# Kernel optimization log

Hardware: AMD Instinct MI355X
Metric: run time of the kernel (lower is better)

The kernel has to match this reference:

```python
import jax, jax.numpy as jnp
import numpy as np

B, ND, NE, D, H = 2, 2048, 2048, 1024, 16
HD = D // H
DFF = 4 * D
EPS = 1e-5


def setup_inputs() -> dict:
    key = jax.random.key(0)
    ks = jax.random.split(key, 16)
    s = lambda fan_in: 1.0 / np.sqrt(fan_in)
    inp = {
        'x': jax.random.normal(ks[0], (B, ND, D), jnp.float32),
        'memory': jax.random.normal(ks[1], (B, NE, D), jnp.float32),
        'ln1_g': jnp.ones((D,), jnp.float32), 'ln1_b': jnp.zeros((D,), jnp.float32),
        'Wqkv': jax.random.normal(ks[2], (D, 3 * D), jnp.float32) * s(D),
        'Wo_sa': jax.random.normal(ks[3], (D, D), jnp.float32) * s(D),
        'bo_sa': jnp.zeros((D,), jnp.float32),
        'ln2_g': jnp.ones((D,), jnp.float32), 'ln2_b': jnp.zeros((D,), jnp.float32),
        'Wq': jax.random.normal(ks[4], (D, D), jnp.float32) * s(D),
        'Wk': jax.random.normal(ks[5], (D, D), jnp.float32) * s(D),
        'Wv': jax.random.normal(ks[6], (D, D), jnp.float32) * s(D),
        'Wo_ca': jax.random.normal(ks[7], (D, D), jnp.float32) * s(D),
        'bo_ca': jnp.zeros((D,), jnp.float32),
        'ln3_g': jnp.ones((D,), jnp.float32), 'ln3_b': jnp.zeros((D,), jnp.float32),
        'W1': jax.random.normal(ks[8], (D, DFF), jnp.float32) * s(D),
        'b1': jnp.zeros((DFF,), jnp.float32),
        'W2': jax.random.normal(ks[9], (DFF, D), jnp.float32) * s(DFF),
        'b2': jnp.zeros((D,), jnp.float32),
        'attn_mask': jnp.tril(jnp.ones((ND, ND), jnp.bool_)),
    }
    return inp


def _layernorm(x, g, b):
    mu = jnp.mean(x, axis=-1, keepdims=True)
    var = jnp.mean(jnp.square(x - mu), axis=-1, keepdims=True)
    return (x - mu) * jax.lax.rsqrt(var + EPS) * g + b


def _heads(t, n):  # (B,N,D) -> (B,H,N,HD)
    Bn = t.shape[0]
    return t.reshape(Bn, n, H, HD).transpose(0, 2, 1, 3)


def _attend(q, k, v, mask=None):
    scale = HD ** -0.5
    scores = jnp.einsum('bhqd,bhkd->bhqk', q, k) * scale
    if mask is not None:
        scores = jnp.where(mask, scores, -jnp.inf)
    attn = jax.nn.softmax(scores, axis=-1)
    out = jnp.einsum('bhqk,bhkd->bhqd', attn, v)
    Bn, _, Nq, _ = out.shape
    return out.transpose(0, 2, 1, 3).reshape(Bn, Nq, D)


def reference(x, memory, ln1_g, ln1_b, Wqkv, Wo_sa, bo_sa, ln2_g, ln2_b,
              Wq, Wk, Wv, Wo_ca, bo_ca, ln3_g, ln3_b, W1, b1, W2, b2, attn_mask):
    # --- masked self-attention ---
    h = _layernorm(x, ln1_g, ln1_b)
    qkv = (h @ Wqkv).reshape(B, ND, 3, H, HD).transpose(2, 0, 3, 1, 4)  # (3,B,H,N,HD)
    q, k, v = qkv[0], qkv[1], qkv[2]
    sa = _attend(q, k, v, attn_mask[None, None]) @ Wo_sa + bo_sa
    x = x + sa
    # --- cross-attention ---
    h = _layernorm(x, ln2_g, ln2_b)
    q = _heads(h @ Wq, ND)
    k = _heads(memory @ Wk, NE)
    v = _heads(memory @ Wv, NE)
    ca = _attend(q, k, v) @ Wo_ca + bo_ca
    x = x + ca
    # --- FFN ---
    h = _layernorm(x, ln3_g, ln3_b)
    x = x + (jax.nn.gelu(h @ W1 + b1, approximate=False) @ W2 + b2)
    return x
```

## Files before the change

### kernel.cpp

```cpp
#include <hip/hip_runtime.h>
#include <hip/hip_bf16.h>
#include <math.h>

#define B_   2
#define ND_  2048
#define NE_  2048
#define D_   1024
#define H_   16
#define HD_  64
#define DFF_ 4096
#define T_   4096

typedef __attribute__((ext_vector_type(8))) short bf16x8;
typedef __attribute__((ext_vector_type(4))) float f32x4;

#if __has_builtin(__builtin_amdgcn_exp2f)
#define EXP2(x) __builtin_amdgcn_exp2f(x)
#else
#define EXP2(x) exp2f(x)
#endif

__device__ __forceinline__ short f2bf(float f) {
  union { float f; unsigned u; } v; v.f = f;
  return (short)((v.u + 0x7FFFu + ((v.u >> 16) & 1u)) >> 16);
}
__device__ __forceinline__ float bf2f(short s) {
  union { unsigned u; float f; } v; v.u = ((unsigned)(unsigned short)s) << 16;
  return v.f;
}

typedef const __attribute__((address_space(1))) void gvoid_t;
typedef __attribute__((address_space(3))) void lvoid_t;

__device__ __forceinline__ void gload16(const void* src, void* dst) {
  __builtin_amdgcn_global_load_lds((gvoid_t*)src, (lvoid_t*)dst, 16, 0, 0);
}

__global__ __launch_bounds__(256) void prep(
    const float* __restrict__ Wqkv, short* __restrict__ wqkv_t,
    const float* __restrict__ W1, short* __restrict__ w1_t,
    const float* __restrict__ W2, short* __restrict__ w2_t,
    const float* __restrict__ i0, const float* __restrict__ i1,
    const float* __restrict__ i2, const float* __restrict__ i3,
    const float* __restrict__ i4,
    short* __restrict__ o0, short* __restrict__ o1, short* __restrict__ o2,
    short* __restrict__ o3, short* __restrict__ o4,
    const float* __restrict__ mem, short* __restrict__ membf) {
  const int id = blockIdx.x;
  const int tid = threadIdx.x;
  if (id >= 16384) {
    const int i = (id - 16384) * 256 + tid;
    float4 v = ((const float4*)mem)[i];
    short4 o;
    o.x = f2bf(v.x); o.y = f2bf(v.y); o.z = f2bf(v.z); o.w = f2bf(v.w);
    ((short4*)membf)[i] = o;
    return;
  }
  const float* in; short* out; int K, N, bx, by;
  if (id < 3072) {
    in = Wqkv; out = wqkv_t; K = 1024; N = 3072; bx = id % 96; by = id / 96;
  } else if (id < 7168) {
    const int t = id - 3072;
    in = W1; out = w1_t; K = 1024; N = 4096; bx = t % 128; by = t / 128;
  } else if (id < 11264) {
    const int t = id - 7168;
    in = W2; out = w2_t; K = 4096; N = 1024; bx = t % 32; by = t / 32;
  } else {
    const int t = id - 11264;
    const int z = t >> 10, r = t & 1023;
    bx = r % 32; by = r / 32; K = 1024; N = 1024;
    in  = z == 0 ? i0 : z == 1 ? i1 : z == 2 ? i2 : z == 3 ? i3 : i4;
    out = z == 0 ? o0 : z == 1 ? o1 : z == 2 ? o2 : z == 3 ? o3 : o4;
  }
  __shared__ float tb[32][33];
  const int tx = tid & 31, ty = tid >> 5;
  const int n0 = bx * 32, k0 = by * 32;
#pragma unroll
  for (int i = 0; i < 4; ++i)
    tb[ty + i * 8][tx] = in[(size_t)(k0 + ty + i * 8) * N + n0 + tx];
  __syncthreads();
#pragma unroll
  for (int i = 0; i < 4; ++i)
    out[(size_t)(n0 + ty + i * 8) * K + k0 + tx] = f2bf(tb[tx][ty + i * 8]);
}

__global__ __launch_bounds__(256) void ln_kernel(const float* __restrict__ x,
                                                 const float* __restrict__ g,
                                                 const float* __restrict__ b,
                                                 short* __restrict__ out) {
  const int row = blockIdx.x;
  const int tid = threadIdx.x;
  const float* xr = x + (size_t)row * D_;
  float4 v = reinterpret_cast<const float4*>(xr)[tid];
  float s  = v.x + v.y + v.z + v.w;
  float s2 = v.x * v.x + v.y * v.y + v.z * v.z + v.w * v.w;
#pragma unroll
  for (int m = 1; m < 64; m <<= 1) {
    s  += __shfl_xor(s, m);
    s2 += __shfl_xor(s2, m);
  }
  __shared__ float ss[4], ss2[4];
  const int w = tid >> 6;
  if ((tid & 63) == 0) { ss[w] = s; ss2[w] = s2; }
  __syncthreads();
  s  = ss[0] + ss[1] + ss[2] + ss[3];
  s2 = ss2[0] + ss2[1] + ss2[2] + ss2[3];
  const float mu   = s * (1.0f / D_);
  const float var  = s2 * (1.0f / D_) - mu * mu;
  const float rstd = rsqrtf(var + 1e-5f);
  float4 gv = reinterpret_cast<const float4*>(g)[tid];
  float4 bv = reinterpret_cast<const float4*>(b)[tid];
  short4 o;
  o.x = f2bf((v.x - mu) * rstd * gv.x + bv.x);
  o.y = f2bf((v.y - mu) * rstd * gv.y + bv.y);
  o.z = f2bf((v.z - mu) * rstd * gv.z + bv.z);
  o.w = f2bf((v.w - mu) * rstd * gv.w + bv.w);
  reinterpret_cast<short4*>(out + (size_t)row * D_)[tid] = o;
}

__global__ __launch_bounds__(256) void ln_fused(const float* __restrict__ xprev,
                                                const short* delta,
                                                const float* __restrict__ pbias,
                                                const float* __restrict__ g,
                                                const float* __restrict__ b,
                                                short* out_ln,
                                                float* __restrict__ out_x) {
  const int row = blockIdx.x;
  const int tid = threadIdx.x;
  float4 v = reinterpret_cast<const float4*>(xprev + (size_t)row * D_)[tid];
  short4 dv = reinterpret_cast<const short4*>(delta + (size_t)row * D_)[tid];
  float4 pb = reinterpret_cast<const float4*>(pbias)[tid];
  v.x += bf2f(dv.x) + pb.x;
  v.y += bf2f(dv.y) + pb.y;
  v.z += bf2f(dv.z) + pb.z;
  v.w += bf2f(dv.w) + pb.w;
  float s  = v.x + v.y + v.z + v.w;
  float s2 = v.x * v.x + v.y * v.y + v.z * v.z + v.w * v.w;
#pragma unroll
  for (int m = 1; m < 64; m <<= 1) {
    s  += __shfl_xor(s, m);
    s2 += __shfl_xor(s2, m);
  }
  __shared__ float ss[4], ss2[4];
  const int w = tid >> 6;
  if ((tid & 63) == 0) { ss[w] = s; ss2[w] = s2; }
  __syncthreads();
  s  = ss[0] + ss[1] + ss[2] + ss[3];
  s2 = ss2[0] + ss2[1] + ss2[2] + ss2[3];
  const float mu   = s * (1.0f / D_);
  const float var  = s2 * (1.0f / D_) - mu * mu;
  const float rstd = rsqrtf(var + 1e-5f);
  reinterpret_cast<float4*>(out_x + (size_t)row * D_)[tid] = v;
  float4 gv = reinterpret_cast<const float4*>(g)[tid];
  float4 bv = reinterpret_cast<const float4*>(b)[tid];
  short4 o;
  o.x = f2bf((v.x - mu) * rstd * gv.x + bv.x);
  o.y = f2bf((v.y - mu) * rstd * gv.y + bv.y);
  o.z = f2bf((v.z - mu) * rstd * gv.z + bv.z);
  o.w = f2bf((v.w - mu) * rstd * gv.w + bv.w);
  reinterpret_cast<short4*>(out_ln + (size_t)row * D_)[tid] = o;
}

__global__ __launch_bounds__(256) void addbias(const float* __restrict__ x,
                                               const short* __restrict__ delta,
                                               const float* __restrict__ bias,
                                               float* __restrict__ out) {
  const int i = blockIdx.x * 256 + threadIdx.x;
  float4 v = ((const float4*)x)[i];
  short4 dv = ((const short4*)delta)[i];
  const int col = (i * 4) & (D_ - 1);
  float4 pb = *(const float4*)(bias + col);
  v.x += bf2f(dv.x) + pb.x;
  v.y += bf2f(dv.y) + pb.y;
  v.z += bf2f(dv.z) + pb.z;
  v.w += bf2f(dv.w) + pb.w;
  ((float4*)out)[i] = v;
}

template <int MODE>
__global__ __launch_bounds__(256) void gemm_bt(const short* __restrict__ A,
                                               const short* __restrict__ Bt,
                                               const float* __restrict__ bias,
                                               void* __restrict__ Cout,
                                               int M, int N, int K) {
  __shared__ short As[2][128 * 64];
  __shared__ short Bs[2][128 * 64];
  const int tid = threadIdx.x;
  const int gx = gridDim.x;
  const int nwg = gx * gridDim.y;
  int lin = blockIdx.y * gx + blockIdx.x;
  lin = (lin & 7) * (nwg >> 3) + (lin >> 3);
  const int m0 = (lin / gx) * 128, n0 = (lin % gx) * 128;
  const int wave = tid >> 6, lane = tid & 63;
  const int wm = (wave >> 1) * 64, wn = (wave & 1) * 64;
  const int lr = lane & 15, lg = lane >> 4;
  const int lx = lr & 7;

  f32x4 acc[4][4];
#pragma unroll
  for (int i = 0; i < 4; ++i)
#pragma unroll
    for (int j = 0; j < 4; ++j) acc[i][j] = f32x4{0.f, 0.f, 0.f, 0.f};

  const int sr = tid >> 3;
  const int scs = ((tid & 7) ^ (sr & 7)) * 8;
  const size_t arow = (size_t)(m0 + sr) * K + scs;
  const size_t brow = (size_t)(n0 + sr) * K + scs;

  auto stage = [&](int buf, int k0) {
#pragma unroll
    for (int p = 0; p < 4; ++p) {
      gload16(A + arow + (size_t)(p * 32) * K + k0, &As[buf][p * 2048 + tid * 8]);
      gload16(Bt + brow + (size_t)(p * 32) * K + k0, &Bs[buf][p * 2048 + tid * 8]);
    }
  };

  stage(0, 0);
  __syncthreads();
  int cur = 0;
  for (int k0 = 0; k0 < K; k0 += 64) {
    if (k0 + 64 < K) stage(cur ^ 1, k0 + 64);
    const short* Ab = &As[cur][0];
    const short* Bb = &Bs[cur][0];
#pragma unroll
    for (int kk = 0; kk < 2; ++kk) {
      bf16x8 af[4], bfr[4];
#pragma unroll
      for (int mi = 0; mi < 4; ++mi)
        af[mi] = *(const bf16x8*)(Ab + (wm + mi * 16 + lr) * 64 +
                                  (((kk * 4 + lg) ^ lx) * 8));
#pragma unroll
      for (int ni = 0; ni < 4; ++ni)
        bfr[ni] = *(const bf16x8*)(Bb + (wn + ni * 16 + lr) * 64 +
                                   (((kk * 4 + lg) ^ lx) * 8));
#pragma unroll
      for (int mi = 0; mi < 4; ++mi)
#pragma unroll
        for (int ni = 0; ni < 4; ++ni)
          acc[mi][ni] = __builtin_amdgcn_mfma_f32_16x16x32_bf16(
              af[mi], bfr[ni], acc[mi][ni], 0, 0, 0);
    }
    __syncthreads();
    cur ^= 1;
  }

#pragma unroll
  for (int mi = 0; mi < 4; ++mi) {
    const int row = m0 + wm + mi * 16 + lg * 4;
#pragma unroll
    for (int ni = 0; ni < 4; ++ni) {
      const int col = n0 + wn + ni * 16 + lr;
#pragma unroll
      for (int r = 0; r < 4; ++r) {
        const size_t idx = (size_t)(row + r) * N + col;
        const float v = acc[mi][ni][r];
        if (MODE == 0) {
          ((short*)Cout)[idx] = f2bf(v);
        } else {
          const float tt = v + bias[col];
          const float yy = fmaf(tt * tt * tt, 0.044715f, tt);
          const float e = EXP2(yy * -2.3022343813918633f);
          ((short*)Cout)[idx] = f2bf(tt / (1.0f + e));
        }
      }
    }
  }
}

__global__ __launch_bounds__(256) void gemm_bt3(const short* __restrict__ A0,
                                                const short* __restrict__ A1,
                                                const short* __restrict__ A2,
                                                const short* __restrict__ B0,
                                                const short* __restrict__ B1,
                                                const short* __restrict__ B2,
                                                short* __restrict__ C0,
                                                short* __restrict__ C1,
                                                short* __restrict__ C2,
                                                int M, int N, int K) {
  const int z = blockIdx.z;
  const short* A  = z == 0 ? A0 : (z == 1 ? A1 : A2);
  const short* Bt = z == 0 ? B0 : (z == 1 ? B1 : B2);
  short* C        = z == 0 ? C0 : (z == 1 ? C1 : C2);

  __shared__ short As[2][128 * 64];
  __shared__ short Bs[2][128 * 64];
  const int tid = threadIdx.x;
  const int gx = gridDim.x;
  const int nwg = gx * gridDim.y;
  int lin = blockIdx.y * gx + blockIdx.x;
  lin = (lin & 7) * (nwg >> 3) + (lin >> 3);
  const int m0 = (lin / gx) * 128, n0 = (lin % gx) * 128;
  const int wave = tid >> 6, lane = tid & 63;
  const int wm = (wave >> 1) * 64, wn = (wave & 1) * 64;
  const int lr = lane & 15, lg = lane >> 4;
  const int lx = lr & 7;

  f32x4 acc[4][4];
#pragma unroll
  for (int i = 0; i < 4; ++i)
#pragma unroll
    for (int j = 0; j < 4; ++j) acc[i][j] = f32x4{0.f, 0.f, 0.f, 0.f};

  const int sr = tid >> 3;
  const int scs = ((tid & 7) ^ (sr & 7)) * 8;
  const size_t arow = (size_t)(m0 + sr) * K + scs;
  const size_t brow = (size_t)(n0 + sr) * K + scs;

  auto stage = [&](int buf, int k0) {
#pragma unroll
    for (int p = 0; p < 4; ++p) {
      gload16(A + arow + (size_t)(p * 32) * K + k0, &As[buf][p * 2048 + tid * 8]);
      gload16(Bt + brow + (size_t)(p * 32) * K + k0, &Bs[buf][p * 2048 + tid * 8]);
    }
  };

  stage(0, 0);
  __syncthreads();
  int cur = 0;
  for (int k0 = 0; k0 < K; k0 += 64) {
    if (k0 + 64 < K) stage(cur ^ 1, k0 + 64);
    const short* Ab = &As[cur][0];
    const short* Bb = &Bs[cur][0];
#pragma unroll
    for (int kk = 0; kk < 2; ++kk) {
      bf16x8 af[4], bfr[4];
#pragma unroll
      for (int mi = 0; mi < 4; ++mi)
        af[mi] = *(const bf16x8*)(Ab + (wm + mi * 16 + lr) * 64 +
                                  (((kk * 4 + lg) ^ lx) * 8));
#pragma unroll
      for (int ni = 0; ni < 4; ++ni)
        bfr[ni] = *(const bf16x8*)(Bb + (wn + ni * 16 + lr) * 64 +
                                   (((kk * 4 + lg) ^ lx) * 8));
#pragma unroll
      for (int mi = 0; mi < 4; ++mi)
#pragma unroll
        for (int ni = 0; ni < 4; ++ni)
          acc[mi][ni] = __builtin_amdgcn_mfma_f32_16x16x32_bf16(
              af[mi], bfr[ni], acc[mi][ni], 0, 0, 0);
    }
    __syncthreads();
    cur ^= 1;
  }

#pragma unroll
  for (int mi = 0; mi < 4; ++mi) {
    const int row = m0 + wm + mi * 16 + lg * 4;
#pragma unroll
    for (int ni = 0; ni < 4; ++ni) {
      const int col = n0 + wn + ni * 16 + lr;
#pragma unroll
      for (int r = 0; r < 4; ++r)
        C[(size_t)(row + r) * N + col] = f2bf(acc[mi][ni][r]);
    }
  }
}

__global__ __launch_bounds__(256) void gemm_bt64(const short* __restrict__ A,
                                                 const short* __restrict__ Bt,
                                                 short* __restrict__ Cout,
                                                 int M, int N, int K) {
  __shared__ short As[2][64 * 64];
  __shared__ short Bs[2][128 * 64];
  const int tid = threadIdx.x;
  const int gx = gridDim.x;
  const int nwg = gx * gridDim.y;
  int lin = blockIdx.y * gx + blockIdx.x;
  lin = (lin & 7) * (nwg >> 3) + (lin >> 3);
  const int m0 = (lin / gx) * 64, n0 = (lin % gx) * 128;
  const int wave = tid >> 6, lane = tid & 63;
  const int wn = wave * 32;
  const int lr = lane & 15, lg = lane >> 4;
  const int lx = lr & 7;

  f32x4 acc[4][2];
#pragma unroll
  for (int i = 0; i < 4; ++i)
#pragma unroll
    for (int j = 0; j < 2; ++j) acc[i][j] = f32x4{0.f, 0.f, 0.f, 0.f};

  const int sr = tid >> 3;
  const int scs = ((tid & 7) ^ (sr & 7)) * 8;
  const size_t arow = (size_t)(m0 + sr) * K + scs;
  const size_t brow = (size_t)(n0 + sr) * K + scs;

  auto stage = [&](int buf, int k0) {
#pragma unroll
    for (int p = 0; p < 2; ++p)
      gload16(A + arow + (size_t)(p * 32) * K + k0, &As[buf][p * 2048 + tid * 8]);
#pragma unroll
    for (int p = 0; p < 4; ++p)
      gload16(Bt + brow + (size_t)(p * 32) * K + k0, &Bs[buf][p * 2048 + tid * 8]);
  };

  stage(0, 0);
  __syncthreads();
  int cur = 0;
  for (int k0 = 0; k0 < K; k0 += 64) {
    if (k0 + 64 < K) stage(cur ^ 1, k0 + 64);
    const short* Ab = &As[cur][0];
    const short* Bb = &Bs[cur][0];
#pragma unroll
    for (int kk = 0; kk < 2; ++kk) {
      bf16x8 af[4], bfr[2];
#pragma unroll
      for (int mi = 0; mi < 4; ++mi)
        af[mi] = *(const bf16x8*)(Ab + (mi * 16 + lr) * 64 +
                                  (((kk * 4 + lg) ^ lx) * 8));
#pragma unroll
      for (int ni = 0; ni < 2; ++ni)
        bfr[ni] = *(const bf16x8*)(Bb + (wn + ni * 16 + lr) * 64 +
                                   (((kk * 4 + lg) ^ lx) * 8));
#pragma unroll
      for (int mi = 0; mi < 4; ++mi)
#pragma unroll
        for (int ni = 0; ni < 2; ++ni)
          acc[mi][ni] = __builtin_amdgcn_mfma_f32_16x16x32_bf16(
              af[mi], bfr[ni], acc[mi][ni], 0, 0, 0);
    }
    __syncthreads();
    cur ^= 1;
  }

#pragma unroll
  for (int mi = 0; mi < 4; ++mi) {
    const int row = m0 + mi * 16 + lg * 4;
#pragma unroll
    for (int ni = 0; ni < 2; ++ni) {
      const int col = n0 + wn + ni * 16 + lr;
#pragma unroll
      for (int r = 0; r < 4; ++r)
        Cout[(size_t)(row + r) * N + col] = f2bf(acc[mi][ni][r]);
    }
  }
}

__global__ __launch_bounds__(256) void vtrans(const short* __restrict__ in,
                                              short* __restrict__ out,
                                              int ldi, int N) {
  const int bh = blockIdx.z;
  const int b = bh >> 4, h = bh & 15;
  const short* ib = in + (size_t)b * N * ldi + h * HD_;
  short* ob = out + (size_t)bh * HD_ * N;
  __shared__ short t[32][33];
  const int tx = threadIdx.x, ty = threadIdx.y;
  const int n0 = blockIdx.x * 32, d0 = blockIdx.y * 32;
#pragma unroll
  for (int i = 0; i < 4; ++i)
    t[ty + i * 8][tx] = ib[(size_t)(n0 + ty + i * 8) * ldi + d0 + tx];
  __syncthreads();
#pragma unroll
  for (int i = 0; i < 4; ++i)
    ob[(size_t)(d0 + ty + i * 8) * N + n0 + tx] = t[tx][ty + i * 8];
}

__global__ __launch_bounds__(512) void flash(const short* __restrict__ Q,
                                             const short* __restrict__ Kp,
                                             const short* __restrict__ Vt,
                                             short* __restrict__ O,
                                             int ldq, int ldk, int ldo,
                                             int NK, int causal) {
  const int bh = blockIdx.x;
  int qb = blockIdx.y;
  if (causal) qb = (qb < 8) ? (2 * qb) : (31 - 2 * qb);
  const int b = bh >> 4, h = bh & 15;
  const int q0 = qb * 128;
  const int tid = threadIdx.x, wave = tid >> 6, lane = tid & 63;
  const int lr = lane & 15, lg = lane >> 4;
  const int lx = lr & 7;

  const short* Qb = Q + (size_t)b * ND_ * ldq + h * HD_;
  const short* Kb = Kp + (size_t)b * NK * ldk + h * HD_;
  const short* Vb = Vt + (size_t)bh * HD_ * NK;
  short* Ob = O + (size_t)b * ND_ * ldo + h * HD_;

  __shared__ short Ks[2][64 * 64];
  __shared__ short Vs[2][64 * 64];
  __shared__ short Ps[8][16 * 64];

  const int qrow = q0 + wave * 16 + lr;
  const bf16x8 qf0 = *(const bf16x8*)(Qb + (size_t)qrow * ldq + lg * 8);
  const bf16x8 qf1 = *(const bf16x8*)(Qb + (size_t)qrow * ldq + 32 + lg * 8);

  const bf16x8 ONES = {0x3F80, 0x3F80, 0x3F80, 0x3F80,
                       0x3F80, 0x3F80, 0x3F80, 0x3F80};

  f32x4 oacc[4];
  f32x4 lacc = f32x4{0.f, 0.f, 0.f, 0.f};
  float m_own = -1e30f;
#pragma unroll
  for (int i = 0; i < 4; ++i) oacc[i] = f32x4{0.f, 0.f, 0.f, 0.f};

  const int sr0 = tid >> 3;
  const int ssw = ((tid & 7) ^ (sr0 & 7)) * 8;
  const int e0 = tid * 8;

  const float SC = 0.18033688011112042f;

  short* Pw = &Ps[wave][0];
  const int pbase = lr * 64 + (lg & 1) * 4;

  auto stage = [&](int buf, int k0) {
    gload16(Kb + (size_t)(k0 + sr0) * ldk + ssw, &Ks[buf][0] + e0);
    gload16(Vb + (size_t)sr0 * NK + k0 + ssw, &Vs[buf][0] + e0);
  };

  const int nkt = causal ? (2 * qb + 2) : (NK / 64);
  stage(0, 0);
  __syncthreads();
  int cur = 0;
  for (int t = 0; t < nkt; ++t) {
    const int k0 = t * 64;
    if (t + 1 < nkt) stage(cur ^ 1, k0 + 64);
    if (!causal || k0 <= q0 + wave * 16 + 15) {
      const short* Ksb = &Ks[cur][0];
      const short* Vsb = &Vs[cur][0];

      f32x4 st[4];
      __builtin_amdgcn_s_setprio(1);
#pragma unroll
      for (int kb = 0; kb < 4; ++kb) {
        const bf16x8 kf0 = *(const bf16x8*)(Ksb + (kb * 16 + lr) * 64 + ((lg ^ lx) * 8));
        const bf16x8 kf1 = *(const bf16x8*)(Ksb + (kb * 16 + lr) * 64 + (((4 + lg) ^ lx) * 8));
        st[kb] = f32x4{0.f, 0.f, 0.f, 0.f};
        st[kb] = __builtin_amdgcn_mfma_f32_16x16x32_bf16(kf0, qf0, st[kb], 0, 0, 0);
        st[kb] = __builtin_amdgcn_mfma_f32_16x16x32_bf16(kf1, qf1, st[kb], 0, 0, 0);
      }
      __builtin_amdgcn_s_setprio(0);
      if (causal && k0 + 63 > q0 + wave * 16) {
#pragma unroll
        for (int kb = 0; kb < 4; ++kb)
#pragma unroll
          for (int r = 0; r < 4; ++r)
            if ((k0 + kb * 16 + lg * 4 + r) > qrow) st[kb][r] = -3.0e38f;
      }

      float rm = fmaxf(st[0][0], st[0][1]);
      asm("v_max3_f32 %0, %1, %2, %3" : "=v"(rm) : "v"(rm), "v"(st[0][2]), "v"(st[0][3]));
      asm("v_max3_f32 %0, %1, %2, %3" : "=v"(rm) : "v"(rm), "v"(st[1][0]), "v"(st[1][1]));
      asm("v_max3_f32 %0, %1, %2, %3" : "=v"(rm) : "v"(rm), "v"(st[1][2]), "v"(st[1][3]));
      asm("v_max3_f32 %0, %1, %2, %3" : "=v"(rm) : "v"(rm), "v"(st[2][0]), "v"(st[2][1]));
      asm("v_max3_f32 %0, %1, %2, %3" : "=v"(rm) : "v"(rm), "v"(st[2][2]), "v"(st[2][3]));
      asm("v_max3_f32 %0, %1, %2, %3" : "=v"(rm) : "v"(rm), "v"(st[3][0]), "v"(st[3][1]));
      asm("v_max3_f32 %0, %1, %2, %3" : "=v"(rm) : "v"(rm), "v"(st[3][2]), "v"(st[3][3]));
      rm = fmaxf(rm, __shfl_xor(rm, 16));
      rm = fmaxf(rm, __shfl_xor(rm, 32));

      if (!__all(rm - m_own <= 44.f)) {
        const float nm = fmaxf(m_own, rm);
        const float fac = EXP2((m_own - nm) * SC);
        m_own = nm;
        const float fr0 = __shfl(fac, (lg << 2) + 0);
        const float fr1 = __shfl(fac, (lg << 2) + 1);
        const float fr2 = __shfl(fac, (lg << 2) + 2);
        const float fr3 = __shfl(fac, (lg << 2) + 3);
#pragma unroll
        for (int db = 0; db < 4; ++db) {
          oacc[db][0] *= fr0; oacc[db][1] *= fr1;
          oacc[db][2] *= fr2; oacc[db][3] *= fr3;
        }
        lacc[0] *= fr0; lacc[1] *= fr1; lacc[2] *= fr2; lacc[3] *= fr3;
      }
      const float nmsc = m_own * SC;
#pragma unroll
      for (int kb = 0; kb < 4; ++kb)
#pragma unroll
        for (int r = 0; r < 4; ++r)
          st[kb][r] = EXP2(fmaf(st[kb][r], SC, -nmsc));

#pragma unroll
      for (int kb = 0; kb < 4; ++kb) {
        union { unsigned u[2]; unsigned long long ull; } pk;
        asm("v_cvt_pk_bf16_f32 %0, %1, %2"
            : "=v"(pk.u[0]) : "v"(st[kb][0]), "v"(st[kb][1]));
        asm("v_cvt_pk_bf16_f32 %0, %1, %2"
            : "=v"(pk.u[1]) : "v"(st[kb][2]), "v"(st[kb][3]));
        const int cs = kb * 2 + (lg >> 1);
        *(unsigned long long*)(Pw + pbase + ((cs ^ lx) * 8)) = pk.ull;
      }
      const bf16x8 pf0 = *(const bf16x8*)(Pw + lr * 64 + ((lg ^ lx) * 8));
      const bf16x8 pf1 = *(const bf16x8*)(Pw + lr * 64 + (((4 + lg) ^ lx) * 8));

      __builtin_amdgcn_s_setprio(1);
#pragma unroll
      for (int db = 0; db < 4; ++db) {
        const bf16x8 vf0 = *(const bf16x8*)(Vsb + (db * 16 + lr) * 64 + ((lg ^ lx) * 8));
        const bf16x8 vf1 = *(const bf16x8*)(Vsb + (db * 16 + lr) * 64 + (((4 + lg) ^ lx) * 8));
        oacc[db] = __builtin_amdgcn_mfma_f32_16x16x32_bf16(pf0, vf0, oacc[db], 0, 0, 0);
        oacc[db] = __builtin_amdgcn_mfma_f32_16x16x32_bf16(pf1, vf1, oacc[db], 0, 0, 0);
      }
      lacc = __builtin_amdgcn_mfma_f32_16x16x32_bf16(pf0, ONES, lacc, 0, 0, 0);
      lacc = __builtin_amdgcn_mfma_f32_16x16x32_bf16(pf1, ONES, lacc, 0, 0, 0);
      __builtin_amdgcn_s_setprio(0);
    }
    __syncthreads();
    cur ^= 1;
  }
#pragma unroll
  for (int db = 0; db < 4; ++db)
#pragma unroll
    for (int r = 0; r < 4; ++r) {
      const int q = q0 + wave * 16 + lg * 4 + r;
      Ob[(size_t)q * ldo + db * 16 + lr] = f2bf(oacc[db][r] / lacc[r]);
    }
}

extern "C" void kernel_launch(void* const* d_in, const int* in_sizes, int n_in,
                              void* d_out, int out_size, void* d_ws, size_t ws_size,
                              hipStream_t stream) {
  const float* x      = (const float*)d_in[0];
  const float* memory = (const float*)d_in[1];
  const float* ln1_g  = (const float*)d_in[2];
  const float* ln1_b  = (const float*)d_in[3];
  const float* Wqkv   = (const float*)d_in[4];
  const float* Wo_sa  = (const float*)d_in[5];
  const float* bo_sa  = (const float*)d_in[6];
  const float* ln2_g  = (const float*)d_in[7];
  const float* ln2_b  = (const float*)d_in[8];
  const float* Wq     = (const float*)d_in[9];
  const float* Wk     = (const float*)d_in[10];
  const float* Wv     = (const float*)d_in[11];
  const float* Wo_ca  = (const float*)d_in[12];
  const float* bo_ca  = (const float*)d_in[13];
  const float* ln3_g  = (const float*)d_in[14];
  const float* ln3_b  = (const float*)d_in[15];
  const float* W1     = (const float*)d_in[16];
  const float* b1     = (const float*)d_in[17];
  const float* W2     = (const float*)d_in[18];
  const float* b2     = (const float*)d_in[19];

  char* ws = (char*)d_ws;
  size_t o = 0;
  auto alloc = [&](size_t bytes) { char* p = ws + o; o += bytes; return p; };
  short* wqkv_t = (short*)alloc((size_t)3072 * 1024 * 2);
  short* wosa_t = (short*)alloc((size_t)1024 * 1024 * 2);
  short* wq_t   = (short*)alloc((size_t)1024 * 1024 * 2);
  short* wk_t   = (short*)alloc((size_t)1024 * 1024 * 2);
  short* wv_t   = (short*)alloc((size_t)1024 * 1024 * 2);
  short* woca_t = (short*)alloc((size_t)1024 * 1024 * 2);
  short* w1_t   = (short*)alloc((size_t)4096 * 1024 * 2);
  short* w2_t   = (short*)alloc((size_t)1024 * 4096 * 2);
  short* hbf    = (short*)alloc((size_t)T_ * 1024 * 2);
  short* bufa   = (short*)alloc((size_t)T_ * 3072 * 2);
  short* vt     = (short*)alloc((size_t)32 * 64 * 2048 * 2);
  short* attn   = (short*)alloc((size_t)T_ * 1024 * 2);
  short* membf  = (short*)alloc((size_t)T_ * 1024 * 2);
  float* x1     = (float*)alloc((size_t)T_ * 1024 * 4);
  float* x2     = (float*)alloc((size_t)T_ * 1024 * 4);
  if (o > ws_size) return;

  short* ffn = bufa;
  short* qca = bufa;
  short* kca = bufa + (size_t)T_ * 1024;
  short* vca = bufa + (size_t)2 * T_ * 1024;

  const dim3 tb(32, 8);

  prep<<<dim3(20480), 256, 0, stream>>>(Wqkv, wqkv_t, W1, w1_t, W2, w2_t,
                                        Wo_sa, Wq, Wk, Wv, Wo_ca,
                                        wosa_t, wq_t, wk_t, wv_t, woca_t,
                                        memory, membf);

  ln_kernel<<<dim3(T_), 256, 0, stream>>>(x, ln1_g, ln1_b, hbf);
  gemm_bt<0><<<dim3(3072 / 128, T_ / 128), 256, 0, stream>>>(
      hbf, wqkv_t, nullptr, bufa, T_, 3072, 1024);
  vtrans<<<dim3(ND_ / 32, HD_ / 32, 32), tb, 0, stream>>>(bufa + 2048, vt, 3072, ND_);
  flash<<<dim3(32, ND_ / 128), 512, 0, stream>>>(
      bufa, bufa + 1024, vt, attn, 3072, 3072, 1024, ND_, 1);
  gemm_bt64<<<dim3(1024 / 128, T_ / 64), 256, 0, stream>>>(
      attn, wosa_t, hbf, T_, 1024, 1024);
  ln_fused<<<dim3(T_), 256, 0, stream>>>(x, hbf, bo_sa, ln2_g, ln2_b, hbf, x1);

  gemm_bt3<<<dim3(1024 / 128, T_ / 128, 3), 256, 0, stream>>>(
      hbf, membf, membf, wq_t, wk_t, wv_t, qca, kca, vca, T_, 1024, 1024);
  vtrans<<<dim3(NE_ / 32, HD_ / 32, 32), tb, 0, stream>>>(vca, vt, 1024, NE_);
  flash<<<dim3(32, ND_ / 128), 512, 0, stream>>>(
      qca, kca, vt, attn, 1024, 1024, 1024, NE_, 0);
  gemm_bt64<<<dim3(1024 / 128, T_ / 64), 256, 0, stream>>>(
      attn, woca_t, hbf, T_, 1024, 1024);
  ln_fused<<<dim3(T_), 256, 0, stream>>>(x1, hbf, bo_ca, ln3_g, ln3_b, hbf, x2);

  gemm_bt<2><<<dim3(4096 / 128, T_ / 128), 256, 0, stream>>>(
      hbf, w1_t, b1, ffn, T_, 4096, 1024);
  gemm_bt64<<<dim3(1024 / 128, T_ / 64), 256, 0, stream>>>(
      ffn, w2_t, hbf, T_, 1024, 4096);
  addbias<<<dim3((T_ * 1024) / (256 * 4)), 256, 0, stream>>>(
      x2, hbf, b2, (float*)d_out);
}
```

Before: 369.3 us.

## Process two 16-row query tiles per wave in flash attention with 256 threads

Each wave in the flash attention kernel now handles 32 query rows as two 16-row sub-tiles, so every K and V fragment read from LDS feeds twice as many MFMAs. The block drops from 8 to 4 waves and each thread stages two K/V chunks instead of one. LDS traffic per FLOP goes down, but register pressure rises and fewer waves are resident per block to hide latency. The setprio hints and the inline max3 asm are also removed, and the causal skip now applies per 32-row group, which is coarser than before.

```diff
diff --git a/kernel.cpp b/kernel.cpp
--- a/kernel.cpp
+++ b/kernel.cpp
@@ -454,7 +454,7 @@
     ob[(size_t)(d0 + ty + i * 8) * N + n0 + tx] = t[tx][ty + i * 8];
 }
 
-__global__ __launch_bounds__(512) void flash(const short* __restrict__ Q,
+__global__ __launch_bounds__(256) void flash(const short* __restrict__ Q,
                                              const short* __restrict__ Kp,
                                              const short* __restrict__ Vt,
                                              short* __restrict__ O,
@@ -478,31 +478,41 @@
   __shared__ short Vs[2][64 * 64];
   __shared__ short Ps[8][16 * 64];
 
-  const int qrow = q0 + wave * 16 + lr;
-  const bf16x8 qf0 = *(const bf16x8*)(Qb + (size_t)qrow * ldq + lg * 8);
-  const bf16x8 qf1 = *(const bf16x8*)(Qb + (size_t)qrow * ldq + 32 + lg * 8);
+  const int qbase = q0 + wave * 32;
+  const int qra = qbase + lr, qrb = qbase + 16 + lr;
+  const bf16x8 qf0a = *(const bf16x8*)(Qb + (size_t)qra * ldq + lg * 8);
+  const bf16x8 qf1a = *(const bf16x8*)(Qb + (size_t)qra * ldq + 32 + lg * 8);
+  const bf16x8 qf0b = *(const bf16x8*)(Qb + (size_t)qrb * ldq + lg * 8);
+  const bf16x8 qf1b = *(const bf16x8*)(Qb + (size_t)qrb * ldq + 32 + lg * 8);
 
   const bf16x8 ONES = {0x3F80, 0x3F80, 0x3F80, 0x3F80,
                        0x3F80, 0x3F80, 0x3F80, 0x3F80};
 
-  f32x4 oacc[4];
-  f32x4 lacc = f32x4{0.f, 0.f, 0.f, 0.f};
-  float m_own = -1e30f;
-#pragma unroll
-  for (int i = 0; i < 4; ++i) oacc[i] = f32x4{0.f, 0.f, 0.f, 0.f};
+  f32x4 oacca[4], oaccb[4];
+  f32x4 lacca = f32x4{0.f, 0.f, 0.f, 0.f};
+  f32x4 laccb = f32x4{0.f, 0.f, 0.f, 0.f};
+  float ma = -1e30f, mb = -1e30f;
+#pragma unroll
+  for (int i = 0; i < 4; ++i) {
+    oacca[i] = f32x4{0.f, 0.f, 0.f, 0.f};
+    oaccb[i] = f32x4{0.f, 0.f, 0.f, 0.f};
+  }
 
   const int sr0 = tid >> 3;
   const int ssw = ((tid & 7) ^ (sr0 & 7)) * 8;
-  const int e0 = tid * 8;
+  const int e0 = tid * 8, e1 = 2048 + tid * 8;
 
   const float SC = 0.18033688011112042f;
 
-  short* Pw = &Ps[wave][0];
+  short* Pwa = &Ps[wave * 2][0];
+  short* Pwb = &Ps[wave * 2 + 1][0];
   const int pbase = lr * 64 + (lg & 1) * 4;
 
   auto stage = [&](int buf, int k0) {
     gload16(Kb + (size_t)(k0 + sr0) * ldk + ssw, &Ks[buf][0] + e0);
+    gload16(Kb + (size_t)(k0 + 32 + sr0) * ldk + ssw, &Ks[buf][0] + e1);
     gload16(Vb + (size_t)sr0 * NK + k0 + ssw, &Vs[buf][0] + e0);
+    gload16(Vb + (size_t)(32 + sr0) * NK + k0 + ssw, &Vs[buf][0] + e1);
   };
 
   const int nkt = causal ? (2 * qb + 2) : (NK / 64);
@@ -512,86 +522,116 @@
   for (int t = 0; t < nkt; ++t) {
     const int k0 = t * 64;
     if (t + 1 < nkt) stage(cur ^ 1, k0 + 64);
-    if (!causal || k0 <= q0 + wave * 16 + 15) {
+    if (!causal || k0 <= qbase + 31) {
       const short* Ksb = &Ks[cur][0];
       const short* Vsb = &Vs[cur][0];
 
-      f32x4 st[4];
-      __builtin_amdgcn_s_setprio(1);
+      f32x4 sa[4], sb[4];
 #pragma unroll
       for (int kb = 0; kb < 4; ++kb) {
         const bf16x8 kf0 = *(const bf16x8*)(Ksb + (kb * 16 + lr) * 64 + ((lg ^ lx) * 8));
         const bf16x8 kf1 = *(const bf16x8*)(Ksb + (kb * 16 + lr) * 64 + (((4 + lg) ^ lx) * 8));
-        st[kb] = f32x4{0.f, 0.f, 0.f, 0.f};
-        st[kb] = __builtin_amdgcn_mfma_f32_16x16x32_bf16(kf0, qf0, st[kb], 0, 0, 0);
-        st[kb] = __builtin_amdgcn_mfma_f32_16x16x32_bf16(kf1, qf1, st[kb], 0, 0, 0);
+        sa[kb] = f32x4{0.f, 0.f, 0.f, 0.f};
+        sb[kb] = f32x4{0.f, 0.f, 0.f, 0.f};
+        sa[kb] = __builtin_amdgcn_mfma_f32_16x16x32_bf16(kf0, qf0a, sa[kb], 0, 0, 0);
+        sa[kb] = __builtin_amdgcn_mfma_f32_16x16x32_bf16(kf1, qf1a, sa[kb], 0, 0, 0);
+        sb[kb] = __builtin_amdgcn_mfma_f32_16x16x32_bf16(kf0, qf0b, sb[kb], 0, 0, 0);
+        sb[kb] = __builtin_amdgcn_mfma_f32_16x16x32_bf16(kf1, qf1b, sb[kb], 0, 0, 0);
       }
-      __builtin_amdgcn_s_setprio(0);
-      if (causal && k0 + 63 > q0 + wave * 16) {
+      if (causal && k0 + 63 > qbase) {
 #pragma unroll
         for (int kb = 0; kb < 4; ++kb)
 #pragma unroll
-          for (int r = 0; r < 4; ++r)
-            if ((k0 + kb * 16 + lg * 4 + r) > qrow) st[kb][r] = -3.0e38f;
+          for (int r = 0; r < 4; ++r) {
+            const int kk = k0 + kb * 16 + lg * 4 + r;
+            if (kk > qra) sa[kb][r] = -3.0e38f;
+            if (kk > qrb) sb[kb][r] = -3.0e38f;
+          }
       }
 
-      float rm = fmaxf(st[0][0], st[0][1]);
-      asm("v_max3_f32 %0, %1, %2, %3" : "=v"(rm) : "v"(rm), "v"(st[0][2]), "v"(st[0][3]));
-      asm("v_max3_f32 %0, %1, %2, %3" : "=v"(rm) : "v"(rm), "v"(st[1][0]), "v"(st[1][1]));
-      asm("v_max3_f32 %0, %1, %2, %3" : "=v"(rm) : "v"(rm), "v"(st[1][2]), "v"(st[1][3]));
-      asm("v_max3_f32 %0, %1, %2, %3" : "=v"(rm) : "v"(rm), "v"(st[2][0]), "v"(st[2][1]));
-      asm("v_max3_f32 %0, %1, %2, %3" : "=v"(rm) : "v"(rm), "v"(st[2][2]), "v"(st[2][3]));
-      asm("v_max3_f32 %0, %1, %2, %3" : "=v"(rm) : "v"(rm), "v"(st[3][0]), "v"(st[3][1]));
-      asm("v_max3_f32 %0, %1, %2, %3" : "=v"(rm) : "v"(rm), "v"(st[3][2]), "v"(st[3][3]));
-      rm = fmaxf(rm, __shfl_xor(rm, 16));
-      rm = fmaxf(rm, __shfl_xor(rm, 32));
-
-      if (!__all(rm - m_own <= 44.f)) {
-        const float nm = fmaxf(m_own, rm);
-        const float fac = EXP2((m_own - nm) * SC);
-        m_own = nm;
-        const float fr0 = __shfl(fac, (lg << 2) + 0);
-        const float fr1 = __shfl(fac, (lg << 2) + 1);
-        const float fr2 = __shfl(fac, (lg << 2) + 2);
-        const float fr3 = __shfl(fac, (lg << 2) + 3);
+      float rma = sa[0][0], rmb = sb[0][0];
+#pragma unroll
+      for (int kb = 0; kb < 4; ++kb)
+#pragma unroll
+        for (int r = 0; r < 4; ++r) {
+          if (kb || r) {
+            rma = fmaxf(rma, sa[kb][r]);
+            rmb = fmaxf(rmb, sb[kb][r]);
+          }
+        }
+      rma = fmaxf(rma, __shfl_xor(rma, 16));
+      rma = fmaxf(rma, __shfl_xor(rma, 32));
+      rmb = fmaxf(rmb, __shfl_xor(rmb, 16));
+      rmb = fmaxf(rmb, __shfl_xor(rmb, 32));
+
+      const int ok = (rma - ma <= 44.f) & (rmb - mb <= 44.f);
+      if (!__all(ok)) {
+        const float nma = fmaxf(ma, rma);
+        const float faca = EXP2((ma - nma) * SC);
+        ma = nma;
+        const float nmb = fmaxf(mb, rmb);
+        const float facb = EXP2((mb - nmb) * SC);
+        mb = nmb;
+        const float fa0 = __shfl(faca, (lg << 2) + 0);
+        const float fa1 = __shfl(faca, (lg << 2) + 1);
+        const float fa2 = __shfl(faca, (lg << 2) + 2);
+        const float fa3 = __shfl(faca, (lg << 2) + 3);
+        const float fb0 = __shfl(facb, (lg << 2) + 0);
+        const float fb1 = __shfl(facb, (lg << 2) + 1);
+        const float fb2 = __shfl(facb, (lg << 2) + 2);
+        const float fb3 = __shfl(facb, (lg << 2) + 3);
 #pragma unroll
         for (int db = 0; db < 4; ++db) {
-          oacc[db][0] *= fr0; oacc[db][1] *= fr1;
-          oacc[db][2] *= fr2; oacc[db][3] *= fr3;
+          oacca[db][0] *= fa0; oacca[db][1] *= fa1;
+          oacca[db][2] *= fa2; oacca[db][3] *= fa3;
+          oaccb[db][0] *= fb0; oaccb[db][1] *= fb1;
+          oaccb[db][2] *= fb2; oaccb[db][3] *= fb3;
         }
-        lacc[0] *= fr0; lacc[1] *= fr1; lacc[2] *= fr2; lacc[3] *= fr3;
+        lacca[0] *= fa0; lacca[1] *= fa1; lacca[2] *= fa2; lacca[3] *= fa3;
+        laccb[0] *= fb0; laccb[1] *= fb1; laccb[2] *= fb2; laccb[3] *= fb3;
       }
-      const float nmsc = m_own * SC;
+      const float nmsa = ma * SC, nmsb = mb * SC;
 #pragma unroll
       for (int kb = 0; kb < 4; ++kb)
 #pragma unroll
-        for (int r = 0; r < 4; ++r)
-          st[kb][r] = EXP2(fmaf(st[kb][r], SC, -nmsc));
+        for (int r = 0; r < 4; ++r) {
+          sa[kb][r] = EXP2(fmaf(sa[kb][r], SC, -nmsa));
+          sb[kb][r] = EXP2(fmaf(sb[kb][r], SC, -nmsb));
+        }
 
 #pragma unroll
       for (int kb = 0; kb < 4; ++kb) {
-        union { unsigned u[2]; unsigned long long ull; } pk;
+        const int cs = kb * 2 + (lg >> 1);
+        union { unsigned u[2]; unsigned long long ull; } pa, pb;
         asm("v_cvt_pk_bf16_f32 %0, %1, %2"
-            : "=v"(pk.u[0]) : "v"(st[kb][0]), "v"(st[kb][1]));
+            : "=v"(pa.u[0]) : "v"(sa[kb][0]), "v"(sa[kb][1]));
         asm("v_cvt_pk_bf16_f32 %0, %1, %2"
-            : "=v"(pk.u[1]) : "v"(st[kb][2]), "v"(st[kb][3]));
-        const int cs = kb * 2 + (lg >> 1);
-        *(unsigned long long*)(Pw + pbase + ((cs ^ lx) * 8)) = pk.ull;
+            : "=v"(pa.u[1]) : "v"(sa[kb][2]), "v"(sa[kb][3]));
+        asm("v_cvt_pk_bf16_f32 %0, %1, %2"
+            : "=v"(pb.u[0]) : "v"(sb[kb][0]), "v"(sb[kb][1]));
+        asm("v_cvt_pk_bf16_f32 %0, %1, %2"
+            : "=v"(pb.u[1]) : "v"(sb[kb][2]), "v"(sb[kb][3]));
+        *(unsigned long long*)(Pwa + pbase + ((cs ^ lx) * 8)) = pa.ull;
+        *(unsigned long long*)(Pwb + pbase + ((cs ^ lx) * 8)) = pb.ull;
       }
-      const bf16x8 pf0 = *(const bf16x8*)(Pw + lr * 64 + ((lg ^ lx) * 8));
-      const bf16x8 pf1 = *(const bf16x8*)(Pw + lr * 64 + (((4 + lg) ^ lx) * 8));
-
-      __builtin_amdgcn_s_setprio(1);
+      const bf16x8 pfa0 = *(const bf16x8*)(Pwa + lr * 64 + ((lg ^ lx) * 8));
+      const bf16x8 pfa1 = *(const bf16x8*)(Pwa + lr * 64 + (((4 + lg) ^ lx) * 8));
+      const bf16x8 pfb0 = *(const bf16x8*)(Pwb + lr * 64 + ((lg ^ lx) * 8));
+      const bf16x8 pfb1 = *(const bf16x8*)(Pwb + lr * 64 + (((4 + lg) ^ lx) * 8));
+
 #pragma unroll
       for (int db = 0; db < 4; ++db) {
         const bf16x8 vf0 = *(const bf16x8*)(Vsb + (db * 16 + lr) * 64 + ((lg ^ lx) * 8));
         const bf16x8 vf1 = *(const bf16x8*)(Vsb + (db * 16 + lr) * 64 + (((4 + lg) ^ lx) * 8));
-        oacc[db] = __builtin_amdgcn_mfma_f32_16x16x32_bf16(pf0, vf0, oacc[db], 0, 0, 0);
-        oacc[db] = __builtin_amdgcn_mfma_f32_16x16x32_bf16(pf1, vf1, oacc[db], 0, 0, 0);
+        oacca[db] = __builtin_amdgcn_mfma_f32_16x16x32_bf16(pfa0, vf0, oacca[db], 0, 0, 0);
+        oacca[db] = __builtin_amdgcn_mfma_f32_16x16x32_bf16(pfa1, vf1, oacca[db], 0, 0, 0);
+        oaccb[db] = __builtin_amdgcn_mfma_f32_16x16x32_bf16(pfb0, vf0, oaccb[db], 0, 0, 0);
+        oaccb[db] = __builtin_amdgcn_mfma_f32_16x16x32_bf16(pfb1, vf1, oaccb[db], 0, 0, 0);
       }
-      lacc = __builtin_amdgcn_mfma_f32_16x16x32_bf16(pf0, ONES, lacc, 0, 0, 0);
-      lacc = __builtin_amdgcn_mfma_f32_16x16x32_bf16(pf1, ONES, lacc, 0, 0, 0);
-      __builtin_amdgcn_s_setprio(0);
+      lacca = __builtin_amdgcn_mfma_f32_16x16x32_bf16(pfa0, ONES, lacca, 0, 0, 0);
+      lacca = __builtin_amdgcn_mfma_f32_16x16x32_bf16(pfa1, ONES, lacca, 0, 0, 0);
+      laccb = __builtin_amdgcn_mfma_f32_16x16x32_bf16(pfb0, ONES, laccb, 0, 0, 0);
+      laccb = __builtin_amdgcn_mfma_f32_16x16x32_bf16(pfb1, ONES, laccb, 0, 0, 0);
     }
     __syncthreads();
     cur ^= 1;
@@ -600,8 +640,10 @@
   for (int db = 0; db < 4; ++db)
 #pragma unroll
     for (int r = 0; r < 4; ++r) {
-      const int q = q0 + wave * 16 + lg * 4 + r;
-      Ob[(size_t)q * ldo + db * 16 + lr] = f2bf(oacc[db][r] / lacc[r]);
+      const int qa = qbase + lg * 4 + r;
+      const int qbq = qbase + 16 + lg * 4 + r;
+      Ob[(size_t)qa * ldo + db * 16 + lr] = f2bf(oacca[db][r] / lacca[r]);
+      Ob[(size_t)qbq * ldo + db * 16 + lr] = f2bf(oaccb[db][r] / laccb[r]);
     }
 }
 
@@ -665,7 +707,7 @@
   gemm_bt<0><<<dim3(3072 / 128, T_ / 128), 256, 0, stream>>>(
       hbf, wqkv_t, nullptr, bufa, T_, 3072, 1024);
   vtrans<<<dim3(ND_ / 32, HD_ / 32, 32), tb, 0, stream>>>(bufa + 2048, vt, 3072, ND_);
-  flash<<<dim3(32, ND_ / 128), 512, 0, stream>>>(
+  flash<<<dim3(32, ND_ / 128), 256, 0, stream>>>(
       bufa, bufa + 1024, vt, attn, 3072, 3072, 1024, ND_, 1);
   gemm_bt64<<<dim3(1024 / 128, T_ / 64), 256, 0, stream>>>(
       attn, wosa_t, hbf, T_, 1024, 1024);
@@ -674,7 +716,7 @@
   gemm_bt3<<<dim3(1024 / 128, T_ / 128, 3), 256, 0, stream>>>(
       hbf, membf, membf, wq_t, wk_t, wv_t, qca, kca, vca, T_, 1024, 1024);
   vtrans<<<dim3(NE_ / 32, HD_ / 32, 32), tb, 0, stream>>>(vca, vt, 1024, NE_);
-  flash<<<dim3(32, ND_ / 128), 512, 0, stream>>>(
+  flash<<<dim3(32, ND_ / 128), 256, 0, stream>>>(
       qca, kca, vt, attn, 1024, 1024, 1024, NE_, 0);
   gemm_bt64<<<dim3(1024 / 128, T_ / 64), 256, 0, stream>>>(
       attn, woca_t, hbf, T_, 1024, 1024);
```

New measurement: 388.2 us. 1.05x slower.
